# Kernel optimization log

Hardware: AMD Instinct MI355X
Metric: run time of the kernel (lower is better)

Reference implementation:

```python
import jax, jax.numpy as jnp
import numpy as np

BN_EPS = 1e-5


def binarize(x):
    # sign binarization with straight-through estimator (identity grad)
    return x + jax.lax.stop_gradient(jnp.sign(x) - x)


def conv2d(x, w, stride):
    # x: [N,C,H,W], w: [O,I,kh,kw], VALID padding (PyTorch default padding=0)
    return jax.lax.conv_general_dilated(
        x, w, window_strides=(stride, stride), padding='VALID',
        dimension_numbers=('NCHW', 'OIHW', 'NCHW'))


def batchnorm(x, gamma, beta, mean, var):
    inv = gamma / jnp.sqrt(var + BN_EPS)          # [C]
    return x * inv[None, :, None, None] + (beta - mean * inv)[None, :, None, None]


def setup_inputs() -> dict:
    key = jax.random.key(0)
    ks = jax.random.split(key, 20)
    B = 8192
    f32 = jnp.float32
    d = {
        'x': jax.random.normal(ks[0], (B, 1, 24, 54), f32),
        'conv1_w': jax.random.normal(ks[1], (32, 1, 3, 3), f32) * 0.3,
        'conv1_b': jax.random.normal(ks[2], (32,), f32) * 0.1,
        'bn1_gamma': 1.0 + 0.1 * jax.random.normal(ks[3], (32,), f32),
        'bn1_beta': 0.1 * jax.random.normal(ks[4], (32,), f32),
        'bn1_mean': 0.1 * jax.random.normal(ks[5], (32,), f32),
        'bn1_var': jax.random.uniform(ks[6], (32,), f32, 0.5, 1.5),
        'conv2_w': jax.random.normal(ks[7], (64, 32, 3, 3), f32) * 0.1,
        'conv2_b': jax.random.normal(ks[8], (64,), f32) * 0.1,
        'bn2_gamma': 1.0 + 0.1 * jax.random.normal(ks[9], (64,), f32),
        'bn2_beta': 0.1 * jax.random.normal(ks[10], (64,), f32),
        'bn2_mean': 0.1 * jax.random.normal(ks[11], (64,), f32),
        'bn2_var': jax.random.uniform(ks[12], (64,), f32, 0.5, 1.5),
        'lin_w': jax.random.normal(ks[13], (500, 3840), f32) * 0.02,
        'lin_b': jax.random.normal(ks[14], (500,), f32) * 0.1,
        'out_w': jax.random.normal(ks[15], (10, 500), f32) * 0.05,
        'out_b': jax.random.normal(ks[16], (10,), f32) * 0.1,
    }
    return d


def reference(x, conv1_w, conv1_b, bn1_gamma, bn1_beta, bn1_mean, bn1_var,
              conv2_w, conv2_b, bn2_gamma, bn2_beta, bn2_mean, bn2_var,
              lin_w, lin_b, out_w, out_b):
    # conv1: input channels (1) != 3 -> input binarized; weight binarized; float bias
    h = conv2d(binarize(x), binarize(conv1_w), 2) + conv1_b[None, :, None, None]
    h = jax.nn.relu(batchnorm(h, bn1_gamma, bn1_beta, bn1_mean, bn1_var))  # [B,32,11,26]
    # conv2: input channels (32) != 3 -> input binarized (values in {0,1} post-ReLU)
    h = conv2d(binarize(h), binarize(conv2_w), 2) + conv2_b[None, :, None, None]
    h = jax.nn.relu(batchnorm(h, bn2_gamma, bn2_beta, bn2_mean, bn2_var))  # [B,64,5,12]
    h = h.reshape(-1, 3840)
    # BinarizeLinear: in_features (3840, 500) != 784 -> input binarized
    h = jax.nn.relu(binarize(h) @ binarize(lin_w).T + lin_b[None, :])      # [B,500]
    y = binarize(h) @ binarize(out_w).T + out_b[None, :]                   # [B,10]
    return y
```

## Files before the change

kernel.cpp:

```cpp
#include <hip/hip_runtime.h>
#include <cstdint>

#define BN_EPS 1e-5f

static constexpr int NB = 8192;
static constexpr int JLIN = 500;

typedef int v4i  __attribute__((ext_vector_type(4)));
typedef int v16i __attribute__((ext_vector_type(16)));


__global__ __launch_bounds__(256) void pack_kernel(
    const float* __restrict__ conv1_w, const float* __restrict__ conv1_b,
    const float* __restrict__ conv2_w, const float* __restrict__ conv2_b,
    const float* __restrict__ lin_w, const float* __restrict__ lin_b,
    const float* __restrict__ out_w,
    const float* __restrict__ bn1_g, const float* __restrict__ bn1_b,
    const float* __restrict__ bn1_m, const float* __restrict__ bn1_v,
    const float* __restrict__ bn2_g, const float* __restrict__ bn2_b,
    const float* __restrict__ bn2_m, const float* __restrict__ bn2_v,
    uint4* __restrict__ wbfrag, uint32_t* __restrict__ cdat,
    uint32_t* __restrict__ lut, uint32_t* __restrict__ wout,
    int* __restrict__ Tlin, uint4* __restrict__ wcfrag)
{
    __shared__ float    s_c1w[288];
    __shared__ uint32_t s_wp[32];
    __shared__ float    s_inv1[32], s_sh1[32], s_b1[32];

    int tid = threadIdx.x;
    int b   = blockIdx.x;

    if (b < 512) {
        int e  = b * 256 + tid;
        int L  = e & 63;
        int kq = (e >> 6) & 127;
        int jt = e >> 13;
        int j  = jt * 32 + (L & 31);
        int h  = L >> 5;
        uint32_t dd[4] = {0u, 0u, 0u, 0u};
        if (j < JLIN) {
            int c  = kq >> 1, hi = kq & 1;
            int nb = (hi ? 28 : 32) - 16 * h;
            const float4* s4 = (const float4*)(lin_w + (size_t)j * 3840 +
                                               c * 60 + hi * 32 + 16 * h);
            float4 q0 = s4[0], q1 = s4[1], q2 = s4[2], q3 = s4[3];
            float qf[16] = {q0.x, q0.y, q0.z, q0.w, q1.x, q1.y, q1.z, q1.w,
                            q2.x, q2.y, q2.z, q2.w, q3.x, q3.y, q3.z, q3.w};
            #pragma unroll
            for (int i = 0; i < 16; ++i) {
                uint32_t byte = (i < nb) ? ((qf[i] > 0.0f) ? 0x01u : 0xFFu) : 0u;
                dd[i >> 2] |= byte << (8 * (i & 3));
            }
        }
        wbfrag[e] = make_uint4(dd[0], dd[1], dd[2], dd[3]);
        return;
    }

    if (b >= 520) {
        int e = (b - 520) * 256 + tid;
        if (e < 1152) {
            int t = e >> 7;
            int n = (e >> 6) & 1;
            int L = e & 63;
            int c = n * 32 + (L & 31);
            int hb = L >> 5;
            bool flip = (bn2_g[c] < 0.0f);
            uint32_t dd[4] = {0u, 0u, 0u, 0u};
            #pragma unroll
            for (int i = 0; i < 16; ++i) {
                int ic = 16 * hb + i;
                float w = conv2_w[c * 288 + ic * 9 + t];
                uint32_t byte = ((w > 0.0f) == flip) ? 0xFFu : 0x01u;
                dd[i >> 2] |= byte << (8 * (i & 3));
            }
            wcfrag[e] = make_uint4(dd[0], dd[1], dd[2], dd[3]);
        }
        return;
    }

    int mb = b - 512;
    if (mb < 2) {
        for (int i = tid; i < 288; i += 256) s_c1w[i] = conv1_w[i];
        __syncthreads();
        if (tid < 32) {
            uint32_t wp = 0;
            for (int t = 0; t < 9; ++t)
                wp |= (s_c1w[tid * 9 + t] < 0.0f ? 1u : 0u) << t;
            s_wp[tid] = wp;
            float inv = bn1_g[tid] / sqrtf(bn1_v[tid] + BN_EPS);
            s_inv1[tid] = inv;
            s_sh1[tid]  = bn1_b[tid] - bn1_m[tid] * inv;
            s_b1[tid]   = conv1_b[tid];
        }
        __syncthreads();
        uint32_t px = (uint32_t)(mb * 256 + tid);
        uint32_t word = 0;
        for (int c = 0; c < 32; ++c) {
            int d = 9 - 2 * __popc(px ^ s_wp[c]);
            float z = __fadd_rn((float)d, s_b1[c]);
            z = __fadd_rn(__fmul_rn(z, s_inv1[c]), s_sh1[c]);
            word |= (z > 0.0f ? 1u : 0u) << c;
        }
        lut[px] = word;
        return;
    }

    int idx = (mb - 2) * 256 + tid;
    if (idx < 576) {
        int c = idx / 9, tap = idx % 9;
        uint32_t w = 0;
        for (int ic = 0; ic < 32; ++ic)
            w |= (conv2_w[c * 288 + ic * 9 + tap] > 0.0f ? 1u : 0u) << ic;
        float inv = bn2_g[c] / sqrtf(bn2_v[c] + BN_EPS);
        if (inv < 0.0f) w = ~w;
        cdat[tap * 64 + c] = w;
    } else if (idx < 576 + 64) {
        int c = idx - 576;
        float inv = bn2_g[c] / sqrtf(bn2_v[c] + BN_EPS);
        float sh  = bn2_b[c] - bn2_m[c] * inv;
        float b2  = conv2_b[c];
        int T = 10000;
        for (int u = -300; u <= 300; ++u) {
            float v = (inv < 0.0f) ? (float)(-u) : (float)u;
            float z = __fadd_rn(__fmul_rn(__fadd_rn(v, b2), inv), sh);
            if (z > 0.0f) { T = u; break; }
        }
        cdat[576 + c] = (uint32_t)T;
    } else if (idx < 576 + 64 + 512) {
        int j = idx - (576 + 64);
        int T = 10000;
        if (j < JLIN) {
            float lb = lin_b[j];
            int base = (int)floorf(-lb) - 2;
            for (int u = base; u <= base + 5; ++u)
                if (__fadd_rn((float)u, lb) > 0.0f) { T = u; break; }
        }
        Tlin[j] = T;
    } else if (idx < 576 + 64 + 512 + 160) {
        int t = idx - (576 + 64 + 512);
        int j = t >> 4, k = t & 15;
        uint32_t w = 0;
        for (int bb = 0; bb < 32; ++bb) {
            int jj = k * 32 + bb;
            if (jj < JLIN) w |= (out_w[j * 500 + jj] > 0.0f ? 1u : 0u) << bb;
        }
        wout[t] = w;
    }
}

__global__ __launch_bounds__(512) void fused_kernel(
    const float* __restrict__ x,
    const uint32_t* __restrict__ cdat,
    const uint32_t* __restrict__ lut,
    const uint4* __restrict__ wcfrag,
    const uint4* __restrict__ wbfrag,
    const int* __restrict__ Tlin,
    const uint32_t* __restrict__ wout,
    const float* __restrict__ out_b,
    float* __restrict__ out)
{
    __shared__ uint32_t s_lut[512];
    __shared__ uint32_t s_wout[160];
    __shared__ __align__(8) uint32_t s_flat[8][44];
    __shared__ uint32_t s_words[8][288];
    __shared__ __align__(8) uint32_t h2w[32][130];
    __shared__ __align__(16) uint8_t As[32 * 520];
    __shared__ uint32_t s_h3[32][16];

    int tid  = threadIdx.x;
    int lane = tid & 63;
    int wv   = tid >> 6;
    int blk  = blockIdx.x;

    s_lut[tid] = lut[tid];
    if (tid < 160) s_wout[tid] = wout[tid];
    __syncthreads();

    int row32 = lane & 31;
    int hb    = lane >> 5;
    int sh_hb = 16 * hb;
    int p1v   = 32 + row32; if (p1v > 59) p1v = 59;
    int wb0, wb1;
    { int oy = row32 / 12, ox = row32 - 12 * oy; wb0 = 52 * oy + 2 * ox; }
    { int oy = p1v / 12,   ox = p1v - 12 * oy;   wb1 = 52 * oy + 2 * ox; }
    int T0 = (int)cdat[576 + row32];
    int T1 = (int)cdat[576 + 32 + row32];

    for (int i = 0; i < 4; ++i) {
        int sl = wv * 4 + i;
        const float* xs = x + ((size_t)blk * 32 + sl) * 1296;

        float xv[21];
        #pragma unroll
        for (int it = 0; it < 21; ++it) {
            int f = it * 64 + lane;
            xv[it] = (f < 1296) ? xs[f] : 1.0f;
        }
        #pragma unroll
        for (int it = 0; it < 21; ++it) {
            uint64_t mk = __ballot(xv[it] < 0.0f);
            if (lane == 0) *(uint64_t*)&s_flat[wv][2 * it] = mk;
        }
        asm volatile("s_waitcnt lgkmcnt(0)" ::: "memory");
        __builtin_amdgcn_sched_barrier(0);

        #pragma unroll
        for (int ii = 0; ii < 5; ++ii) {
            int wnd = ii * 64 + lane;
            if (wnd < 286) {
                int oy = wnd / 26, ox = wnd - 26 * oy;
                uint32_t pxb = 0;
                #pragma unroll
                for (int ky = 0; ky < 3; ++ky) {
                    int bitpos = 54 * (2 * oy + ky) + 2 * ox;
                    int d = bitpos >> 5, sh = bitpos & 31;
                    uint64_t wp = (uint64_t)s_flat[wv][d] |
                                  ((uint64_t)s_flat[wv][d + 1] << 32);
                    pxb |= (((uint32_t)(wp >> sh)) & 7u) << (3 * ky);
                }
                s_words[wv][wnd] = s_lut[pxb];
            }
        }
        asm volatile("s_waitcnt lgkmcnt(0)" ::: "memory");
        __builtin_amdgcn_sched_barrier(0);

        v16i acc[2][2] = {};
        #pragma unroll
        for (int t = 0; t < 9; ++t) {
            const int koff = (t / 3) * 26 + (t % 3);
            uint4 b0 = wcfrag[t * 128 + lane];
            uint4 b1 = wcfrag[t * 128 + 64 + lane];
            v4i bf0 = {(int)b0.x, (int)b0.y, (int)b0.z, (int)b0.w};
            v4i bf1 = {(int)b1.x, (int)b1.y, (int)b1.z, (int)b1.w};
            #pragma unroll
            for (int rt = 0; rt < 2; ++rt) {
                uint32_t w  = s_words[wv][(rt ? wb1 : wb0) + koff];
                uint32_t hw = w >> sh_hb;
                v4i af;
                af[0] = (int)((((hw      ) & 0xFu) * 0x204081u) & 0x01010101u);
                af[1] = (int)((((hw >> 4 ) & 0xFu) * 0x204081u) & 0x01010101u);
                af[2] = (int)((((hw >> 8 ) & 0xFu) * 0x204081u) & 0x01010101u);
                af[3] = (int)((((hw >> 12) & 0xFu) * 0x204081u) & 0x01010101u);
                acc[rt][0] = __builtin_amdgcn_mfma_i32_32x32x32_i8(af, bf0, acc[rt][0], 0, 0, 0);
                acc[rt][1] = __builtin_amdgcn_mfma_i32_32x32x32_i8(af, bf1, acc[rt][1], 0, 0, 0);
            }
        }

        {
            uint32_t w_rt[2];
            #pragma unroll
            for (int rt = 0; rt < 2; ++rt) {
                uint32_t lw0 = 0, lw1 = 0;
                #pragma unroll
                for (int r = 0; r < 16; ++r) {
                    const uint32_t pb = 1u << ((r & 3) + 8 * (r >> 2));
                    if (acc[rt][0][r] >= T0) lw0 |= pb;
                    if (acc[rt][1][r] >= T1) lw1 |= pb;
                }
                lw0 <<= 4 * hb;
                lw1 <<= 4 * hb;
                uint32_t send = hb ? lw0 : lw1;
                uint32_t recv = (uint32_t)__shfl_xor((int)send, 32);
                w_rt[rt] = recv | (hb ? lw1 : lw0);
            }
            uint32_t w0 = w_rt[0];
            uint32_t w1 = w_rt[1] & 0x0FFFFFFFu;
            *(uint2*)&h2w[sl][2 * lane] = make_uint2(w0, w1);
        }
    }
    __syncthreads();

    int jt0 = wv, jt1 = wv + 8;
    int Ta = Tlin[jt0 * 32 + row32];
    int Tb = Tlin[jt1 * 32 + row32];
    int smx = tid >> 4, wlx = tid & 15;

    v16i acc0 = {};
    v16i acc1 = {};

    for (int chunk = 0; chunk < 8; ++chunk) {
        {
            uint32_t w = h2w[smx][chunk * 16 + wlx];
            uint32_t dw[8];
            #pragma unroll
            for (int q = 0; q < 8; ++q)
                dw[q] = (((w >> (4 * q)) & 0xFu) * 0x204081u) & 0x01010101u;
            uint64_t* dst = (uint64_t*)(As + smx * 520 + wlx * 32);
            dst[0] = (uint64_t)dw[0] | ((uint64_t)dw[1] << 32);
            dst[1] = (uint64_t)dw[2] | ((uint64_t)dw[3] << 32);
            dst[2] = (uint64_t)dw[4] | ((uint64_t)dw[5] << 32);
            dst[3] = (uint64_t)dw[6] | ((uint64_t)dw[7] << 32);
        }
        __syncthreads();

        const uint4* b0p = wbfrag + ((size_t)jt0 * 128 + chunk * 16) * 64 + lane;
        const uint4* b1p = wbfrag + ((size_t)jt1 * 128 + chunk * 16) * 64 + lane;
        #pragma unroll 4
        for (int kq = 0; kq < 16; ++kq) {
            uint4 bw0 = b0p[kq * 64];
            uint4 bw1 = b1p[kq * 64];
            v4i bf0 = {(int)bw0.x, (int)bw0.y, (int)bw0.z, (int)bw0.w};
            v4i bf1 = {(int)bw1.x, (int)bw1.y, (int)bw1.z, (int)bw1.w};
            const uint8_t* ap = As + row32 * 520 + kq * 32 + hb * 16;
            uint64_t lo0 = *(const uint64_t*)ap;
            uint64_t hi0 = *(const uint64_t*)(ap + 8);
            v4i a0 = {(int)(uint32_t)lo0, (int)(lo0 >> 32),
                      (int)(uint32_t)hi0, (int)(hi0 >> 32)};
            acc0 = __builtin_amdgcn_mfma_i32_32x32x32_i8(a0, bf0, acc0, 0, 0, 0);
            acc1 = __builtin_amdgcn_mfma_i32_32x32x32_i8(a0, bf1, acc1, 0, 0, 0);
        }
        __syncthreads();
    }

    #pragma unroll
    for (int r = 0; r < 16; ++r) {
        int row0 = (r & 3) + 8 * (r >> 2);
        uint64_t mk0 = __ballot(acc0[r] >= Ta);
        uint64_t mk1 = __ballot(acc1[r] >= Tb);
        if (lane == 0) {
            s_h3[row0][jt0]     = (uint32_t)mk0;
            s_h3[row0 + 4][jt0] = (uint32_t)(mk0 >> 32);
            s_h3[row0][jt1]     = (uint32_t)mk1;
            s_h3[row0 + 4][jt1] = (uint32_t)(mk1 >> 32);
        }
    }
    __syncthreads();

    if (tid < 320) {
        int sl = tid / 10, o = tid - 10 * sl;
        int B = 0, P = 0;
        #pragma unroll
        for (int k = 0; k < 16; ++k) {
            uint32_t w = s_h3[sl][k];
            B += __popc(w);
            P += __popc(w & s_wout[o * 16 + k]);
        }
        out[((size_t)blk * 32 + sl) * 10 + o] = __fadd_rn((float)(2 * P - B), out_b[o]);
    }
}

extern "C" void kernel_launch(void* const* d_in, const int* in_sizes, int n_in,
                              void* d_out, int out_size, void* d_ws, size_t ws_size,
                              hipStream_t stream)
{
    const float* x       = (const float*)d_in[0];
    const float* conv1_w = (const float*)d_in[1];
    const float* conv1_b = (const float*)d_in[2];
    const float* bn1_g   = (const float*)d_in[3];
    const float* bn1_b   = (const float*)d_in[4];
    const float* bn1_m   = (const float*)d_in[5];
    const float* bn1_v   = (const float*)d_in[6];
    const float* conv2_w = (const float*)d_in[7];
    const float* conv2_b = (const float*)d_in[8];
    const float* bn2_g   = (const float*)d_in[9];
    const float* bn2_b   = (const float*)d_in[10];
    const float* bn2_m   = (const float*)d_in[11];
    const float* bn2_v   = (const float*)d_in[12];
    const float* lin_w   = (const float*)d_in[13];
    const float* lin_b   = (const float*)d_in[14];
    const float* out_w   = (const float*)d_in[15];
    const float* out_b   = (const float*)d_in[16];

    char* ws = (char*)d_ws;
    uint4*    wbfrag = (uint4*)   (ws + 4194304);
    uint32_t* cdat   = (uint32_t*)(ws + 6815744);
    uint32_t* lut    = (uint32_t*)(ws + 6818304);
    uint32_t* wout   = (uint32_t*)(ws + 6820352);
    int*      Tlin   = (int*)     (ws + 6820992);
    uint4*    wcfrag = (uint4*)   (ws + 6855808);

    pack_kernel<<<525, 256, 0, stream>>>(conv1_w, conv1_b, conv2_w, conv2_b,
                                         lin_w, lin_b, out_w,
                                         bn1_g, bn1_b, bn1_m, bn1_v,
                                         bn2_g, bn2_b, bn2_m, bn2_v,
                                         wbfrag, cdat, lut, wout, Tlin, wcfrag);
    fused_kernel<<<256, 512, 0, stream>>>(x, cdat, lut, wcfrag, wbfrag,
                                          Tlin, wout, out_b, (float*)d_out);
}
```

Before: 165.6 us.

## Double block to 1024 threads, one linear tile per wave, prefetch both samples

The fused kernel now runs 16 waves per block instead of 8. In the conv stage each wave handles 2 samples instead of 4, and the input loads for both samples are issued up front so memory latency overlaps. In the linear stage each wave owns a single 32-column output tile instead of two. Conv accumulation is reordered per row-tile to reduce live accumulator registers. The aim is more latency hiding from extra waves, at the cost of tighter register limits under 1024-thread launch bounds and larger LDS arrays.

```diff
diff --git a/kernel.cpp b/kernel.cpp
--- a/kernel.cpp
+++ b/kernel.cpp
@@ -148,7 +148,7 @@
     }
 }
 
-__global__ __launch_bounds__(512) void fused_kernel(
+__global__ __launch_bounds__(1024) void fused_kernel(
     const float* __restrict__ x,
     const uint32_t* __restrict__ cdat,
     const uint32_t* __restrict__ lut,
@@ -161,8 +161,8 @@
 {
     __shared__ uint32_t s_lut[512];
     __shared__ uint32_t s_wout[160];
-    __shared__ __align__(8) uint32_t s_flat[8][44];
-    __shared__ uint32_t s_words[8][288];
+    __shared__ __align__(8) uint32_t s_flat[16][44];
+    __shared__ uint32_t s_words[16][288];
     __shared__ __align__(8) uint32_t h2w[32][130];
     __shared__ __align__(16) uint8_t As[32 * 520];
     __shared__ uint32_t s_h3[32][16];
@@ -172,7 +172,7 @@
     int wv   = tid >> 6;
     int blk  = blockIdx.x;
 
-    s_lut[tid] = lut[tid];
+    if (tid < 512) s_lut[tid] = lut[tid];
     if (tid < 160) s_wout[tid] = wout[tid];
     __syncthreads();
 
@@ -186,19 +186,28 @@
     int T0 = (int)cdat[576 + row32];
     int T1 = (int)cdat[576 + 32 + row32];
 
-    for (int i = 0; i < 4; ++i) {
-        int sl = wv * 4 + i;
-        const float* xs = x + ((size_t)blk * 32 + sl) * 1296;
-
-        float xv[21];
+    const float* xsa = x + ((size_t)blk * 32 + wv * 2) * 1296;
+    const float* xsb = xsa + 1296;
+    float xva[21], xvb[21];
+    #pragma unroll
+    for (int it = 0; it < 21; ++it) {
+        int f = it * 64 + lane;
+        xva[it] = (f < 1296) ? xsa[f] : 1.0f;
+    }
+    #pragma unroll
+    for (int it = 0; it < 21; ++it) {
+        int f = it * 64 + lane;
+        xvb[it] = (f < 1296) ? xsb[f] : 1.0f;
+    }
+
+    #pragma unroll
+    for (int i = 0; i < 2; ++i) {
+        int sl = wv * 2 + i;
+
         #pragma unroll
         for (int it = 0; it < 21; ++it) {
-            int f = it * 64 + lane;
-            xv[it] = (f < 1296) ? xs[f] : 1.0f;
-        }
-        #pragma unroll
-        for (int it = 0; it < 21; ++it) {
-            uint64_t mk = __ballot(xv[it] < 0.0f);
+            float v = i ? xvb[it] : xva[it];
+            uint64_t mk = __ballot(v < 0.0f);
             if (lane == 0) *(uint64_t*)&s_flat[wv][2 * it] = mk;
         }
         asm volatile("s_waitcnt lgkmcnt(0)" ::: "memory");
@@ -224,62 +233,53 @@
         asm volatile("s_waitcnt lgkmcnt(0)" ::: "memory");
         __builtin_amdgcn_sched_barrier(0);
 
-        v16i acc[2][2] = {};
+        uint32_t w_rt[2];
         #pragma unroll
-        for (int t = 0; t < 9; ++t) {
-            const int koff = (t / 3) * 26 + (t % 3);
-            uint4 b0 = wcfrag[t * 128 + lane];
-            uint4 b1 = wcfrag[t * 128 + 64 + lane];
-            v4i bf0 = {(int)b0.x, (int)b0.y, (int)b0.z, (int)b0.w};
-            v4i bf1 = {(int)b1.x, (int)b1.y, (int)b1.z, (int)b1.w};
-            #pragma unroll
-            for (int rt = 0; rt < 2; ++rt) {
-                uint32_t w  = s_words[wv][(rt ? wb1 : wb0) + koff];
+        for (int rt = 0; rt < 2; ++rt) {
+            const int wb = rt ? wb1 : wb0;
+            v16i a0 = {};
+            v16i a1 = {};
+            #pragma unroll
+            for (int t = 0; t < 9; ++t) {
+                const int koff = (t / 3) * 26 + (t % 3);
+                uint4 b0 = wcfrag[t * 128 + lane];
+                uint4 b1 = wcfrag[t * 128 + 64 + lane];
+                v4i bf0 = {(int)b0.x, (int)b0.y, (int)b0.z, (int)b0.w};
+                v4i bf1 = {(int)b1.x, (int)b1.y, (int)b1.z, (int)b1.w};
+                uint32_t w  = s_words[wv][wb + koff];
                 uint32_t hw = w >> sh_hb;
                 v4i af;
                 af[0] = (int)((((hw      ) & 0xFu) * 0x204081u) & 0x01010101u);
                 af[1] = (int)((((hw >> 4 ) & 0xFu) * 0x204081u) & 0x01010101u);
                 af[2] = (int)((((hw >> 8 ) & 0xFu) * 0x204081u) & 0x01010101u);
                 af[3] = (int)((((hw >> 12) & 0xFu) * 0x204081u) & 0x01010101u);
-                acc[rt][0] = __builtin_amdgcn_mfma_i32_32x32x32_i8(af, bf0, acc[rt][0], 0, 0, 0);
-                acc[rt][1] = __builtin_amdgcn_mfma_i32_32x32x32_i8(af, bf1, acc[rt][1], 0, 0, 0);
-            }
-        }
-
-        {
-            uint32_t w_rt[2];
-            #pragma unroll
-            for (int rt = 0; rt < 2; ++rt) {
-                uint32_t lw0 = 0, lw1 = 0;
-                #pragma unroll
-                for (int r = 0; r < 16; ++r) {
-                    const uint32_t pb = 1u << ((r & 3) + 8 * (r >> 2));
-                    if (acc[rt][0][r] >= T0) lw0 |= pb;
-                    if (acc[rt][1][r] >= T1) lw1 |= pb;
-                }
-                lw0 <<= 4 * hb;
-                lw1 <<= 4 * hb;
-                uint32_t send = hb ? lw0 : lw1;
-                uint32_t recv = (uint32_t)__shfl_xor((int)send, 32);
-                w_rt[rt] = recv | (hb ? lw1 : lw0);
-            }
-            uint32_t w0 = w_rt[0];
-            uint32_t w1 = w_rt[1] & 0x0FFFFFFFu;
-            *(uint2*)&h2w[sl][2 * lane] = make_uint2(w0, w1);
-        }
+                a0 = __builtin_amdgcn_mfma_i32_32x32x32_i8(af, bf0, a0, 0, 0, 0);
+                a1 = __builtin_amdgcn_mfma_i32_32x32x32_i8(af, bf1, a1, 0, 0, 0);
+            }
+            uint32_t lw0 = 0, lw1 = 0;
+            #pragma unroll
+            for (int r = 0; r < 16; ++r) {
+                const uint32_t pb = 1u << ((r & 3) + 8 * (r >> 2));
+                if (a0[r] >= T0) lw0 |= pb;
+                if (a1[r] >= T1) lw1 |= pb;
+            }
+            lw0 <<= 4 * hb;
+            lw1 <<= 4 * hb;
+            uint32_t send = hb ? lw0 : lw1;
+            uint32_t recv = (uint32_t)__shfl_xor((int)send, 32);
+            w_rt[rt] = recv | (hb ? lw1 : lw0);
+        }
+        *(uint2*)&h2w[sl][2 * lane] = make_uint2(w_rt[0], w_rt[1] & 0x0FFFFFFFu);
     }
     __syncthreads();
 
-    int jt0 = wv, jt1 = wv + 8;
-    int Ta = Tlin[jt0 * 32 + row32];
-    int Tb = Tlin[jt1 * 32 + row32];
+    int jt = wv;
+    int T  = Tlin[jt * 32 + row32];
     int smx = tid >> 4, wlx = tid & 15;
 
-    v16i acc0 = {};
-    v16i acc1 = {};
-
+    v16i acc = {};
     for (int chunk = 0; chunk < 8; ++chunk) {
-        {
+        if (tid < 512) {
             uint32_t w = h2w[smx][chunk * 16 + wlx];
             uint32_t dw[8];
             #pragma unroll
@@ -293,21 +293,17 @@
         }
         __syncthreads();
 
-        const uint4* b0p = wbfrag + ((size_t)jt0 * 128 + chunk * 16) * 64 + lane;
-        const uint4* b1p = wbfrag + ((size_t)jt1 * 128 + chunk * 16) * 64 + lane;
+        const uint4* bp = wbfrag + ((size_t)jt * 128 + chunk * 16) * 64 + lane;
         #pragma unroll 4
         for (int kq = 0; kq < 16; ++kq) {
-            uint4 bw0 = b0p[kq * 64];
-            uint4 bw1 = b1p[kq * 64];
-            v4i bf0 = {(int)bw0.x, (int)bw0.y, (int)bw0.z, (int)bw0.w};
-            v4i bf1 = {(int)bw1.x, (int)bw1.y, (int)bw1.z, (int)bw1.w};
+            uint4 bw = bp[kq * 64];
+            v4i bf = {(int)bw.x, (int)bw.y, (int)bw.z, (int)bw.w};
             const uint8_t* ap = As + row32 * 520 + kq * 32 + hb * 16;
             uint64_t lo0 = *(const uint64_t*)ap;
             uint64_t hi0 = *(const uint64_t*)(ap + 8);
             v4i a0 = {(int)(uint32_t)lo0, (int)(lo0 >> 32),
                       (int)(uint32_t)hi0, (int)(hi0 >> 32)};
-            acc0 = __builtin_amdgcn_mfma_i32_32x32x32_i8(a0, bf0, acc0, 0, 0, 0);
-            acc1 = __builtin_amdgcn_mfma_i32_32x32x32_i8(a0, bf1, acc1, 0, 0, 0);
+            acc = __builtin_amdgcn_mfma_i32_32x32x32_i8(a0, bf, acc, 0, 0, 0);
         }
         __syncthreads();
     }
@@ -315,13 +311,10 @@
     #pragma unroll
     for (int r = 0; r < 16; ++r) {
         int row0 = (r & 3) + 8 * (r >> 2);
-        uint64_t mk0 = __ballot(acc0[r] >= Ta);
-        uint64_t mk1 = __ballot(acc1[r] >= Tb);
+        uint64_t mk = __ballot(acc[r] >= T);
         if (lane == 0) {
-            s_h3[row0][jt0]     = (uint32_t)mk0;
-            s_h3[row0 + 4][jt0] = (uint32_t)(mk0 >> 32);
-            s_h3[row0][jt1]     = (uint32_t)mk1;
-            s_h3[row0 + 4][jt1] = (uint32_t)(mk1 >> 32);
+            s_h3[row0][jt]     = (uint32_t)mk;
+            s_h3[row0 + 4][jt] = (uint32_t)(mk >> 32);
         }
     }
     __syncthreads();
@@ -374,6 +367,6 @@
                                          bn1_g, bn1_b, bn1_m, bn1_v,
                                          bn2_g, bn2_b, bn2_m, bn2_v,
                                          wbfrag, cdat, lut, wout, Tlin, wcfrag);
-    fused_kernel<<<256, 512, 0, stream>>>(x, cdat, lut, wcfrag, wbfrag,
-                                          Tlin, wout, out_b, (float*)d_out);
+    fused_kernel<<<256, 1024, 0, stream>>>(x, cdat, lut, wcfrag, wbfrag,
+                                           Tlin, wout, out_b, (float*)d_out);
 }
```

Measured after the change: 172.4 us. 4.1% more time.

## Pack linear weights as bits and expand to int8 MFMA fragments in registers

Applied to the files above, without the earlier changes.

Linear-layer weights are now stored as 16-bit sign masks instead of 16-byte int8 fragments, and both the A and B operands are expanded from bits to int8 in registers right before each MFMA. This removes the shared-memory A staging buffer and its per-chunk barriers, and cuts global weight traffic by 8x. It also software-prefetches the next sample's input rows during conv processing. The cost is extra ALU bit-expansion work per MFMA and higher register pressure from the prefetch buffer. Padding handling changes: out-of-range K bits now expand to -1 instead of 0, which relies on the A bits being zero there.

```diff
diff --git a/kernel.cpp b/kernel.cpp
--- a/kernel.cpp
+++ b/kernel.cpp
@@ -19,7 +19,7 @@
     const float* __restrict__ bn1_m, const float* __restrict__ bn1_v,
     const float* __restrict__ bn2_g, const float* __restrict__ bn2_b,
     const float* __restrict__ bn2_m, const float* __restrict__ bn2_v,
-    uint4* __restrict__ wbfrag, uint32_t* __restrict__ cdat,
+    uint16_t* __restrict__ wbbith, uint32_t* __restrict__ cdat,
     uint32_t* __restrict__ lut, uint32_t* __restrict__ wout,
     int* __restrict__ Tlin, uint4* __restrict__ wcfrag)
 {
@@ -37,22 +37,19 @@
         int jt = e >> 13;
         int j  = jt * 32 + (L & 31);
         int h  = L >> 5;
-        uint32_t dd[4] = {0u, 0u, 0u, 0u};
+        uint32_t bits = 0;
         if (j < JLIN) {
-            int c  = kq >> 1, hi = kq & 1;
-            int nb = (hi ? 28 : 32) - 16 * h;
             const float4* s4 = (const float4*)(lin_w + (size_t)j * 3840 +
-                                               c * 60 + hi * 32 + 16 * h);
+                                               (kq >> 1) * 60 + (kq & 1) * 32 + 16 * h);
             float4 q0 = s4[0], q1 = s4[1], q2 = s4[2], q3 = s4[3];
             float qf[16] = {q0.x, q0.y, q0.z, q0.w, q1.x, q1.y, q1.z, q1.w,
                             q2.x, q2.y, q2.z, q2.w, q3.x, q3.y, q3.z, q3.w};
             #pragma unroll
-            for (int i = 0; i < 16; ++i) {
-                uint32_t byte = (i < nb) ? ((qf[i] > 0.0f) ? 0x01u : 0xFFu) : 0u;
-                dd[i >> 2] |= byte << (8 * (i & 3));
-            }
-        }
-        wbfrag[e] = make_uint4(dd[0], dd[1], dd[2], dd[3]);
+            for (int i = 0; i < 16; ++i)
+                if (!(qf[i] > 0.0f)) bits |= 1u << i;
+        }
+        wbbith[((size_t)(jt * 64 + (kq >> 1)) * 64 + L) * 2 + (kq & 1)] =
+            (uint16_t)bits;
         return;
     }
 
@@ -153,7 +150,7 @@
     const uint32_t* __restrict__ cdat,
     const uint32_t* __restrict__ lut,
     const uint4* __restrict__ wcfrag,
-    const uint4* __restrict__ wbfrag,
+    const uint32_t* __restrict__ wbbit,
     const int* __restrict__ Tlin,
     const uint32_t* __restrict__ wout,
     const float* __restrict__ out_b,
@@ -164,7 +161,6 @@
     __shared__ __align__(8) uint32_t s_flat[8][44];
     __shared__ uint32_t s_words[8][288];
     __shared__ __align__(8) uint32_t h2w[32][130];
-    __shared__ __align__(16) uint8_t As[32 * 520];
     __shared__ uint32_t s_h3[32][16];
 
     int tid  = threadIdx.x;
@@ -176,7 +172,7 @@
     if (tid < 160) s_wout[tid] = wout[tid];
     __syncthreads();
 
-    int row32 = lane & 31;
+    int row32 = lane & 63 & 31;
     int hb    = lane >> 5;
     int sh_hb = 16 * hb;
     int p1v   = 32 + row32; if (p1v > 59) p1v = 59;
@@ -186,16 +182,28 @@
     int T0 = (int)cdat[576 + row32];
     int T1 = (int)cdat[576 + 32 + row32];
 
+    const float* xs0 = x + ((size_t)blk * 32 + wv * 4) * 1296;
+    float xv[21];
+    #pragma unroll
+    for (int it = 0; it < 21; ++it) {
+        int f = it * 64 + lane;
+        xv[it] = (f < 1296) ? xs0[f] : 1.0f;
+    }
+
+    #pragma unroll
     for (int i = 0; i < 4; ++i) {
         int sl = wv * 4 + i;
-        const float* xs = x + ((size_t)blk * 32 + sl) * 1296;
-
-        float xv[21];
-        #pragma unroll
-        for (int it = 0; it < 21; ++it) {
-            int f = it * 64 + lane;
-            xv[it] = (f < 1296) ? xs[f] : 1.0f;
-        }
+
+        float xvn[21];
+        if (i < 3) {
+            const float* xn = xs0 + (size_t)(i + 1) * 1296;
+            #pragma unroll
+            for (int it = 0; it < 21; ++it) {
+                int f = it * 64 + lane;
+                xvn[it] = (f < 1296) ? xn[f] : 1.0f;
+            }
+        }
+
         #pragma unroll
         for (int it = 0; it < 21; ++it) {
             uint64_t mk = __ballot(xv[it] < 0.0f);
@@ -263,9 +271,12 @@
                 uint32_t recv = (uint32_t)__shfl_xor((int)send, 32);
                 w_rt[rt] = recv | (hb ? lw1 : lw0);
             }
-            uint32_t w0 = w_rt[0];
-            uint32_t w1 = w_rt[1] & 0x0FFFFFFFu;
-            *(uint2*)&h2w[sl][2 * lane] = make_uint2(w0, w1);
+            *(uint2*)&h2w[sl][2 * lane] = make_uint2(w_rt[0], w_rt[1] & 0x0FFFFFFFu);
+        }
+
+        if (i < 3) {
+            #pragma unroll
+            for (int it = 0; it < 21; ++it) xv[it] = xvn[it];
         }
     }
     __syncthreads();
@@ -273,43 +284,38 @@
     int jt0 = wv, jt1 = wv + 8;
     int Ta = Tlin[jt0 * 32 + row32];
     int Tb = Tlin[jt1 * 32 + row32];
-    int smx = tid >> 4, wlx = tid & 15;
+    const uint32_t* bb0 = wbbit + (size_t)jt0 * 64 * 64 + lane;
+    const uint32_t* bb1 = wbbit + (size_t)jt1 * 64 * 64 + lane;
 
     v16i acc0 = {};
     v16i acc1 = {};
-
-    for (int chunk = 0; chunk < 8; ++chunk) {
-        {
-            uint32_t w = h2w[smx][chunk * 16 + wlx];
-            uint32_t dw[8];
-            #pragma unroll
-            for (int q = 0; q < 8; ++q)
-                dw[q] = (((w >> (4 * q)) & 0xFu) * 0x204081u) & 0x01010101u;
-            uint64_t* dst = (uint64_t*)(As + smx * 520 + wlx * 32);
-            dst[0] = (uint64_t)dw[0] | ((uint64_t)dw[1] << 32);
-            dst[1] = (uint64_t)dw[2] | ((uint64_t)dw[3] << 32);
-            dst[2] = (uint64_t)dw[4] | ((uint64_t)dw[5] << 32);
-            dst[3] = (uint64_t)dw[6] | ((uint64_t)dw[7] << 32);
-        }
-        __syncthreads();
-
-        const uint4* b0p = wbfrag + ((size_t)jt0 * 128 + chunk * 16) * 64 + lane;
-        const uint4* b1p = wbfrag + ((size_t)jt1 * 128 + chunk * 16) * 64 + lane;
-        #pragma unroll 4
-        for (int kq = 0; kq < 16; ++kq) {
-            uint4 bw0 = b0p[kq * 64];
-            uint4 bw1 = b1p[kq * 64];
-            v4i bf0 = {(int)bw0.x, (int)bw0.y, (int)bw0.z, (int)bw0.w};
-            v4i bf1 = {(int)bw1.x, (int)bw1.y, (int)bw1.z, (int)bw1.w};
-            const uint8_t* ap = As + row32 * 520 + kq * 32 + hb * 16;
-            uint64_t lo0 = *(const uint64_t*)ap;
-            uint64_t hi0 = *(const uint64_t*)(ap + 8);
-            v4i a0 = {(int)(uint32_t)lo0, (int)(lo0 >> 32),
-                      (int)(uint32_t)hi0, (int)(hi0 >> 32)};
-            acc0 = __builtin_amdgcn_mfma_i32_32x32x32_i8(a0, bf0, acc0, 0, 0, 0);
-            acc1 = __builtin_amdgcn_mfma_i32_32x32x32_i8(a0, bf1, acc1, 0, 0, 0);
-        }
-        __syncthreads();
+    #pragma unroll 4
+    for (int kqp = 0; kqp < 64; ++kqp) {
+        uint32_t bw0 = bb0[kqp * 64];
+        uint32_t bw1 = bb1[kqp * 64];
+        uint2 awp = *(const uint2*)&h2w[row32][2 * kqp];
+        #pragma unroll
+        for (int hf = 0; hf < 2; ++hf) {
+            uint32_t aw = hf ? awp.y : awp.x;
+            uint32_t hw = aw >> sh_hb;
+            v4i af;
+            af[0] = (int)((((hw      ) & 0xFu) * 0x204081u) & 0x01010101u);
+            af[1] = (int)((((hw >> 4 ) & 0xFu) * 0x204081u) & 0x01010101u);
+            af[2] = (int)((((hw >> 8 ) & 0xFu) * 0x204081u) & 0x01010101u);
+            af[3] = (int)((((hw >> 12) & 0xFu) * 0x204081u) & 0x01010101u);
+            uint32_t s0 = hf ? (bw0 >> 16) : (bw0 & 0xFFFFu);
+            uint32_t s1 = hf ? (bw1 >> 16) : (bw1 & 0xFFFFu);
+            v4i bf0, bf1;
+            #pragma unroll
+            for (int q = 0; q < 4; ++q) {
+                uint32_t b01 = (((s0 >> (4 * q)) & 0xFu) * 0x204081u) & 0x01010101u;
+                bf0[q] = (int)(b01 * 0xFEu + 0x01010101u);
+                uint32_t c01 = (((s1 >> (4 * q)) & 0xFu) * 0x204081u) & 0x01010101u;
+                bf1[q] = (int)(c01 * 0xFEu + 0x01010101u);
+            }
+            acc0 = __builtin_amdgcn_mfma_i32_32x32x32_i8(af, bf0, acc0, 0, 0, 0);
+            acc1 = __builtin_amdgcn_mfma_i32_32x32x32_i8(af, bf1, acc1, 0, 0, 0);
+        }
     }
 
     #pragma unroll
@@ -362,7 +368,7 @@
     const float* out_b   = (const float*)d_in[16];
 
     char* ws = (char*)d_ws;
-    uint4*    wbfrag = (uint4*)   (ws + 4194304);
+    uint32_t* wbbit  = (uint32_t*)(ws + 0);
     uint32_t* cdat   = (uint32_t*)(ws + 6815744);
     uint32_t* lut    = (uint32_t*)(ws + 6818304);
     uint32_t* wout   = (uint32_t*)(ws + 6820352);
@@ -373,7 +379,8 @@
                                          lin_w, lin_b, out_w,
                                          bn1_g, bn1_b, bn1_m, bn1_v,
                                          bn2_g, bn2_b, bn2_m, bn2_v,
-                                         wbfrag, cdat, lut, wout, Tlin, wcfrag);
-    fused_kernel<<<256, 512, 0, stream>>>(x, cdat, lut, wcfrag, wbfrag,
+                                         (uint16_t*)wbbit, cdat, lut, wout,
+                                         Tlin, wcfrag);
+    fused_kernel<<<256, 512, 0, stream>>>(x, cdat, lut, wcfrag, wbbit,
                                           Tlin, wout, out_b, (float*)d_out);
 }
```

Result: no change. 164.9 us (-0.4%).
